# Performance work log

Hardware: AMD Instinct MI355X
Metric: run time of the kernel (lower is better)

The kernel has to match this reference:

```python
import jax, jax.numpy as jnp
import numpy as np

DIM = 64
NUM_NODES = 64
SEQ_LEN = 256
BATCH = 64


def setup_inputs() -> dict:
    key = jax.random.key(0)
    ks = jax.random.split(key, 8)
    D = DIM
    x = jax.random.normal(ks[0], (SEQ_LEN, BATCH, NUM_NODES, D), dtype=jnp.float32)
    mask = jnp.ones((SEQ_LEN,), dtype=jnp.int32)
    # msg MLP: Linear(3D -> D) + GELU
    lim_msg = 1.0 / np.sqrt(3 * D)
    msg_W = jax.random.uniform(ks[1], (D, 3 * D), minval=-lim_msg, maxval=lim_msg, dtype=jnp.float32)
    msg_b = jax.random.uniform(ks[2], (D,), minval=-lim_msg, maxval=lim_msg, dtype=jnp.float32)
    # GRUCell(input=D, hidden=D); torch init U(-1/sqrt(hidden), 1/sqrt(hidden))
    lim_g = 1.0 / np.sqrt(D)
    W_ih = jax.random.uniform(ks[3], (3 * D, D), minval=-lim_g, maxval=lim_g, dtype=jnp.float32)
    W_hh = jax.random.uniform(ks[4], (3 * D, D), minval=-lim_g, maxval=lim_g, dtype=jnp.float32)
    b_ih = jax.random.uniform(ks[5], (3 * D,), minval=-lim_g, maxval=lim_g, dtype=jnp.float32)
    b_hh = jax.random.uniform(ks[6], (3 * D,), minval=-lim_g, maxval=lim_g, dtype=jnp.float32)
    # TimeEncode params
    basis_freq = jnp.asarray(1.0 / 10.0 ** np.linspace(0, 9, D), dtype=jnp.float32)
    phase = jnp.zeros((D,), dtype=jnp.float32)
    return {"x": x, "mask": mask, "msg_W": msg_W, "msg_b": msg_b,
            "W_ih": W_ih, "W_hh": W_hh, "b_ih": b_ih, "b_hh": b_hh,
            "basis_freq": basis_freq, "phase": phase}


def _forward(x, mask, msg_W, msg_b, W_ih, W_hh, b_ih, b_hh, basis_freq, phase):
    T, B, C, D = x.shape
    # TimeEncode: cos(t * freq + phase) -> [T, D]
    ts = jnp.arange(T, dtype=jnp.float32)[:, None]
    t_enc = jnp.cos(ts * basis_freq[None, :] + phase[None, :])
    # init_func == 'mean': mean over time -> [B, C, D] -> [B*C, D]
    s0 = jnp.mean(x, axis=0).reshape(B * C, D)
    # time_range = arange(T) * mask (gather indices)
    tr = jnp.arange(T) * mask.astype(jnp.int32)
    x_seq = x[tr].reshape(T, B * C, D)      # gathered timesteps
    te_seq = t_enc[tr]                       # [T, D]

    def step(s, inp):
        xt, tt = inp                        # xt: [B*C, D], tt: [D]
        tt_b = jnp.broadcast_to(tt[None, :], xt.shape)
        cat = jnp.concatenate([xt, s, tt_b], axis=-1)  # [B*C, 3D]
        msg = jax.nn.gelu(cat @ msg_W.T + msg_b, approximate=False)
        # GRUCell (torch gate order: r, z, n)
        gi = msg @ W_ih.T + b_ih
        gh = s @ W_hh.T + b_hh
        i_r, i_z, i_n = jnp.split(gi, 3, axis=-1)
        h_r, h_z, h_n = jnp.split(gh, 3, axis=-1)
        r = jax.nn.sigmoid(i_r + h_r)
        z = jax.nn.sigmoid(i_z + h_z)
        n = jnp.tanh(i_n + r * h_n)
        s_new = (1.0 - z) * n + z * s
        return s_new, s_new

    _, states = jax.lax.scan(step, s0, (x_seq, te_seq))
    return states.reshape(T, B, C, D)


def reference(x, mask, msg_W, msg_b, W_ih, W_hh, b_ih, b_hh, basis_freq, phase):
    return _forward(x, mask, msg_W, msg_b, W_ih, W_hh, b_ih, b_hh, basis_freq, phase)
```

## Files before the change

### kernel.cpp

```cpp
#include <hip/hip_runtime.h>
#include <math.h>

#define DD    64
#define TT    256
#define NROW  4096
#define BLK   512
#define GRID  256

typedef __attribute__((ext_vector_type(8))) short  short8;
typedef __attribute__((ext_vector_type(4))) float  f32x4;

__device__ __forceinline__ unsigned short f2bf(float f) {
  unsigned u = __builtin_bit_cast(unsigned, f);
  u += 0x7fffu + ((u >> 16) & 1u);
  return (unsigned short)(u >> 16);
}

__device__ __forceinline__ unsigned long long pack4(float4 v) {
  return (unsigned long long)f2bf(v.x)
       | ((unsigned long long)f2bf(v.y) << 16)
       | ((unsigned long long)f2bf(v.z) << 32)
       | ((unsigned long long)f2bf(v.w) << 48);
}

__device__ __forceinline__ short8 load_wfrag(const float* p) {
  float4 a = *(const float4*)p;
  float4 b = *(const float4*)(p + 4);
  short8 r;
  r[0] = (short)f2bf(a.x); r[1] = (short)f2bf(a.y);
  r[2] = (short)f2bf(a.z); r[3] = (short)f2bf(a.w);
  r[4] = (short)f2bf(b.x); r[5] = (short)f2bf(b.y);
  r[6] = (short)f2bf(b.z); r[7] = (short)f2bf(b.w);
  return r;
}

__device__ __forceinline__ float fsigmoid(float x) {
  return __builtin_amdgcn_rcpf(1.0f + __expf(-x));
}
__device__ __forceinline__ float ftanh(float x) {
  return 1.0f - 2.0f * __builtin_amdgcn_rcpf(1.0f + __expf(2.0f * x));
}
__device__ __forceinline__ float ferf(float x) {
  float ax = fabsf(x);
  float t  = __builtin_amdgcn_rcpf(fmaf(0.3275911f, ax, 1.0f));
  float p  = fmaf(1.061405429f, t, -1.453152027f);
  p = fmaf(p, t, 1.421413741f);
  p = fmaf(p, t, -0.284496736f);
  p = fmaf(p, t, 0.254829592f);
  p = p * t;
  float y = 1.0f - p * __expf(-ax * ax);
  return copysignf(y, x);
}

__global__ void bias_kernel(const float* __restrict__ msg_W,
                            const float* __restrict__ msg_b,
                            const float* __restrict__ freq,
                            const float* __restrict__ phase,
                            float* __restrict__ bias_t) {
  __shared__ float teL[DD];
  const int t = blockIdx.x;
  const int j = threadIdx.x;
  teL[j] = cosf(fmaf((float)t, freq[j], phase[j]));
  __syncthreads();
  float acc = msg_b[j];
  const float* wrow = msg_W + j * 192 + 128;
  #pragma unroll 8
  for (int k = 0; k < DD; ++k) acc = fmaf(teL[k], wrow[k], acc);
  bias_t[t * DD + j] = acc;
}

__launch_bounds__(BLK, 1)
__global__ void scan4(const float* __restrict__ x,
                      const int*   __restrict__ mask,
                      const float* __restrict__ msg_W,
                      const float* __restrict__ W_ih,
                      const float* __restrict__ W_hh,
                      const float* __restrict__ b_ih,
                      const float* __restrict__ b_hh,
                      const float* __restrict__ bias_t,
                      float* __restrict__ out) {
  __shared__ alignas(16) unsigned short xs[16 * 72];
  __shared__ alignas(16) unsigned short ss[16 * 72];
  __shared__ alignas(16) unsigned short ms[16 * 72];
  __shared__ alignas(16) float s0a[16 * 68];
  __shared__ alignas(16) float ghl[16 * 260];
  __shared__ int tr_lds[TT];

  const int tid  = threadIdx.x;
  const int lane = tid & 63;
  const int wv   = tid >> 6;
  const int grp  = wv >> 2;
  const int w4   = wv & 3;
  const int col  = lane & 15;
  const int kh   = lane >> 4;
  const int n    = w4 * 16 + col;
  const int row0 = blockIdx.x * 16;

  if (tid < TT) tr_lds[tid] = tid * mask[tid];

  short8 wm[4], wi[3][2], wh[3][2];
  float bsum01[2] = {0.f, 0.f}, bih2 = 0.f, bhh2 = 0.f;
  if (grp == 0) {
    const float* mrow = msg_W + (size_t)n * 192;
    #pragma unroll
    for (int kf = 0; kf < 4; ++kf) wm[kf] = load_wfrag(mrow + kf * 32 + kh * 8);
    #pragma unroll
    for (int p = 0; p < 3; ++p) {
      const float* irow = W_ih + (size_t)(p * 64 + n) * 64;
      #pragma unroll
      for (int kf = 0; kf < 2; ++kf) wi[p][kf] = load_wfrag(irow + kf * 32 + kh * 8);
    }
    bsum01[0] = b_ih[n]      + b_hh[n];
    bsum01[1] = b_ih[64 + n] + b_hh[64 + n];
    bih2 = b_ih[128 + n];
    bhh2 = b_hh[128 + n];
  } else {
    #pragma unroll
    for (int p = 0; p < 3; ++p) {
      const float* hrow = W_hh + (size_t)(p * 64 + n) * 64;
      #pragma unroll
      for (int kf = 0; kf < 2; ++kf) wh[p][kf] = load_wfrag(hrow + kf * 32 + kh * 8);
    }
  }

  {
    const int half = tid >> 8, rem = tid & 255;
    const int fr = rem >> 4, fd = (rem & 15) * 4;
    const float* px = x + ((size_t)half * 128) * (NROW * DD)
                        + (size_t)(row0 + fr) * DD + fd;
    float4 acc = {0.f, 0.f, 0.f, 0.f};
    #pragma unroll 4
    for (int tl = 0; tl < 128; ++tl) {
      float4 v = *(const float4*)(px + (size_t)tl * (NROW * DD));
      acc.x += v.x; acc.y += v.y; acc.z += v.z; acc.w += v.w;
    }
    float* dst = (half == 0) ? &s0a[fr * 68 + fd] : &ghl[fr * 68 + fd];
    *(float4*)dst = acc;
  }
  __syncthreads();
  if (tid < 256) {
    const int fr = tid >> 4, fd = (tid & 15) * 4;
    float4 a = *(const float4*)&s0a[fr * 68 + fd];
    float4 b = *(const float4*)&ghl[fr * 68 + fd];
    const float inv = 1.0f / 256.0f;
    float4 m = { (a.x + b.x) * inv, (a.y + b.y) * inv,
                 (a.z + b.z) * inv, (a.w + b.w) * inv };
    *(float4*)&s0a[fr * 68 + fd] = m;
    *(unsigned long long*)&ss[fr * 72 + fd] = pack4(m);
    float4 xv0 = *(const float4*)(x + (size_t)(row0 + fr) * DD + fd);
    *(unsigned long long*)&xs[fr * 72 + fd] = pack4(xv0);
  }
  __syncthreads();

  float s_reg[4] = {0.f, 0.f, 0.f, 0.f};
  float btc = 0.f;
  if (grp == 0) {
    #pragma unroll
    for (int i = 0; i < 4; ++i) s_reg[i] = s0a[(kh * 4 + i) * 68 + n];
    btc = bias_t[n];
    __builtin_amdgcn_s_setprio(1);
  }

  const int t1  = tid & 255;
  const int fr1 = t1 >> 4;
  const int fd1 = (t1 & 15) * 4;
  float4 xv = {0.f, 0.f, 0.f, 0.f};

  for (int t = 0; t < TT; ++t) {
    const int tn = (t + 1 < TT) ? tr_lds[t + 1] : 0;
    if (grp == 0) {
      const unsigned short* ax = &xs[(lane & 15) * 72];
      const unsigned short* as = &ss[(lane & 15) * 72];
      short8 xa0 = *(const short8*)(ax + kh * 8);
      short8 xa1 = *(const short8*)(ax + 32 + kh * 8);
      short8 sa0 = *(const short8*)(as + kh * 8);
      short8 sa1 = *(const short8*)(as + 32 + kh * 8);
      f32x4 accm = {0.f, 0.f, 0.f, 0.f};
      accm = __builtin_amdgcn_mfma_f32_16x16x32_bf16(xa0, wm[0], accm, 0, 0, 0);
      accm = __builtin_amdgcn_mfma_f32_16x16x32_bf16(xa1, wm[1], accm, 0, 0, 0);
      accm = __builtin_amdgcn_mfma_f32_16x16x32_bf16(sa0, wm[2], accm, 0, 0, 0);
      accm = __builtin_amdgcn_mfma_f32_16x16x32_bf16(sa1, wm[3], accm, 0, 0, 0);
      float btn = 0.f;
      if (t + 1 < TT) btn = bias_t[tn * DD + n];
      #pragma unroll
      for (int i = 0; i < 4; ++i) {
        float a = accm[i] + btc;
        float g = 0.5f * a * (1.0f + ferf(a * 0.70710678118654752f));
        ms[(kh * 4 + i) * 72 + n] = f2bf(g);
      }
      btc = btn;
    } else {
      const unsigned short* as = &ss[(lane & 15) * 72];
      short8 sa0 = *(const short8*)(as + kh * 8);
      short8 sa1 = *(const short8*)(as + 32 + kh * 8);
      f32x4 agh[3];
      #pragma unroll
      for (int p = 0; p < 3; ++p) {
        f32x4 c = {0.f, 0.f, 0.f, 0.f};
        c = __builtin_amdgcn_mfma_f32_16x16x32_bf16(sa0, wh[p][0], c, 0, 0, 0);
        c = __builtin_amdgcn_mfma_f32_16x16x32_bf16(sa1, wh[p][1], c, 0, 0, 0);
        agh[p] = c;
      }
      #pragma unroll
      for (int i = 0; i < 4; ++i) {
        float4 gv = { agh[0][i], agh[1][i], agh[2][i], 0.f };
        *(float4*)&ghl[(kh * 4 + i) * 260 + n * 4] = gv;
      }
      if (t > 0) {
        float4 ov = *(const float4*)&s0a[fr1 * 68 + fd1];
        *(float4*)(out + ((size_t)(t - 1) * NROW + row0 + fr1) * DD + fd1) = ov;
      }
      if (t + 1 < TT)
        xv = *(const float4*)(x + ((size_t)tn * NROW + row0 + fr1) * DD + fd1);
    }
    __syncthreads();

    if (grp == 0) {
      const unsigned short* am = &ms[(lane & 15) * 72];
      short8 ma0 = *(const short8*)(am + kh * 8);
      short8 ma1 = *(const short8*)(am + 32 + kh * 8);
      f32x4 agi[3];
      #pragma unroll
      for (int p = 0; p < 3; ++p) {
        f32x4 c = {0.f, 0.f, 0.f, 0.f};
        c = __builtin_amdgcn_mfma_f32_16x16x32_bf16(ma0, wi[p][0], c, 0, 0, 0);
        c = __builtin_amdgcn_mfma_f32_16x16x32_bf16(ma1, wi[p][1], c, 0, 0, 0);
        agi[p] = c;
      }
      #pragma unroll
      for (int i = 0; i < 4; ++i) {
        const int rr = kh * 4 + i;
        float4 gh4 = *(const float4*)&ghl[rr * 260 + n * 4];
        float gr  = agi[0][i] + gh4.x + bsum01[0];
        float gz  = agi[1][i] + gh4.y + bsum01[1];
        float gni = agi[2][i] + bih2;
        float gnh = gh4.z + bhh2;
        float rg = fsigmoid(gr);
        float zg = fsigmoid(gz);
        float ng = ftanh(fmaf(rg, gnh, gni));
        float sn = fmaf(zg, s_reg[i] - ng, ng);
        s_reg[i] = sn;
        ss[rr * 72 + n]  = f2bf(sn);
        s0a[rr * 68 + n] = sn;
      }
    } else {
      if (t + 1 < TT)
        *(unsigned long long*)&xs[fr1 * 72 + fd1] = pack4(xv);
    }
    __syncthreads();
  }

  if (grp == 1) {
    float4 ov = *(const float4*)&s0a[fr1 * 68 + fd1];
    *(float4*)(out + ((size_t)(TT - 1) * NROW + row0 + fr1) * DD + fd1) = ov;
  }
}

extern "C" void kernel_launch(void* const* d_in, const int* in_sizes, int n_in,
                              void* d_out, int out_size, void* d_ws, size_t ws_size,
                              hipStream_t stream) {
  const float* x      = (const float*)d_in[0];
  const int*   mask   = (const int*)  d_in[1];
  const float* msg_W  = (const float*)d_in[2];
  const float* msg_b  = (const float*)d_in[3];
  const float* W_ih   = (const float*)d_in[4];
  const float* W_hh   = (const float*)d_in[5];
  const float* b_ih   = (const float*)d_in[6];
  const float* b_hh   = (const float*)d_in[7];
  const float* freq   = (const float*)d_in[8];
  const float* phase  = (const float*)d_in[9];
  float* out    = (float*)d_out;
  float* bias_t = (float*)d_ws;

  (void)in_sizes; (void)n_in; (void)out_size; (void)ws_size;

  bias_kernel<<<TT, DD, 0, stream>>>(msg_W, msg_b, freq, phase, bias_t);
  scan4<<<GRID, BLK, 0, stream>>>(x, mask, msg_W, W_ih, W_hh,
                                  b_ih, b_hh, bias_t, out);
}
```

Before: 305.2 us.

## Double-buffer x tile, prefetch two steps ahead, and use lgkm-only barriers

The x tile in shared memory becomes double-buffered so the helper wave group can write step t+1's tile and issue the global load for step t+2 before its recurrent matmul. The loop barriers are replaced by a custom barrier that waits only on LDS/scalar counters, so outstanding global loads and stores no longer stall each step. The output is now written directly from registers by the GRU waves instead of being staged through s0a and stored a step later. The message matmul is split into two independent accumulator chains to shorten the MFMA dependency chain. In exchange, the direct output stores are scalar per-lane writes, and correctness now depends on the manual waitcnt handling.

```diff
diff --git a/kernel.cpp b/kernel.cpp
--- a/kernel.cpp
+++ b/kernel.cpp
@@ -9,6 +9,13 @@
 
 typedef __attribute__((ext_vector_type(8))) short  short8;
 typedef __attribute__((ext_vector_type(4))) float  f32x4;
+
+#define BARRIER() do {                                        \
+    asm volatile("s_waitcnt lgkmcnt(0)" ::: "memory");        \
+    __builtin_amdgcn_sched_barrier(0);                        \
+    __builtin_amdgcn_s_barrier();                             \
+    __builtin_amdgcn_sched_barrier(0);                        \
+  } while (0)
 
 __device__ __forceinline__ unsigned short f2bf(float f) {
   unsigned u = __builtin_bit_cast(unsigned, f);
@@ -70,7 +77,7 @@
 }
 
 __launch_bounds__(BLK, 1)
-__global__ void scan4(const float* __restrict__ x,
+__global__ void scan5(const float* __restrict__ x,
                       const int*   __restrict__ mask,
                       const float* __restrict__ msg_W,
                       const float* __restrict__ W_ih,
@@ -79,12 +86,12 @@
                       const float* __restrict__ b_hh,
                       const float* __restrict__ bias_t,
                       float* __restrict__ out) {
-  __shared__ alignas(16) unsigned short xs[16 * 72];
+  __shared__ alignas(16) unsigned short xs[2][16 * 72];
   __shared__ alignas(16) unsigned short ss[16 * 72];
   __shared__ alignas(16) unsigned short ms[16 * 72];
   __shared__ alignas(16) float s0a[16 * 68];
   __shared__ alignas(16) float ghl[16 * 260];
-  __shared__ int tr_lds[TT];
+  __shared__ int tr_lds[TT + 2];
 
   const int tid  = threadIdx.x;
   const int lane = tid & 63;
@@ -97,6 +104,7 @@
   const int row0 = blockIdx.x * 16;
 
   if (tid < TT) tr_lds[tid] = tid * mask[tid];
+  else if (tid < TT + 2) tr_lds[tid] = 0;
 
   short8 wm[4], wi[3][2], wh[3][2];
   float bsum01[2] = {0.f, 0.f}, bih2 = 0.f, bhh2 = 0.f;
@@ -148,7 +156,7 @@
     *(float4*)&s0a[fr * 68 + fd] = m;
     *(unsigned long long*)&ss[fr * 72 + fd] = pack4(m);
     float4 xv0 = *(const float4*)(x + (size_t)(row0 + fr) * DD + fd);
-    *(unsigned long long*)&xs[fr * 72 + fd] = pack4(xv0);
+    *(unsigned long long*)&xs[0][fr * 72 + fd] = pack4(xv0);
   }
   __syncthreads();
 
@@ -165,31 +173,37 @@
   const int fr1 = t1 >> 4;
   const int fd1 = (t1 & 15) * 4;
   float4 xv = {0.f, 0.f, 0.f, 0.f};
+  if (grp == 1)
+    xv = *(const float4*)(x + ((size_t)tr_lds[1] * NROW + row0 + fr1) * DD + fd1);
 
   for (int t = 0; t < TT; ++t) {
-    const int tn = (t + 1 < TT) ? tr_lds[t + 1] : 0;
     if (grp == 0) {
-      const unsigned short* ax = &xs[(lane & 15) * 72];
+      const unsigned short* ax = &xs[t & 1][(lane & 15) * 72];
       const unsigned short* as = &ss[(lane & 15) * 72];
       short8 xa0 = *(const short8*)(ax + kh * 8);
       short8 xa1 = *(const short8*)(ax + 32 + kh * 8);
       short8 sa0 = *(const short8*)(as + kh * 8);
       short8 sa1 = *(const short8*)(as + 32 + kh * 8);
-      f32x4 accm = {0.f, 0.f, 0.f, 0.f};
-      accm = __builtin_amdgcn_mfma_f32_16x16x32_bf16(xa0, wm[0], accm, 0, 0, 0);
-      accm = __builtin_amdgcn_mfma_f32_16x16x32_bf16(xa1, wm[1], accm, 0, 0, 0);
-      accm = __builtin_amdgcn_mfma_f32_16x16x32_bf16(sa0, wm[2], accm, 0, 0, 0);
-      accm = __builtin_amdgcn_mfma_f32_16x16x32_bf16(sa1, wm[3], accm, 0, 0, 0);
       float btn = 0.f;
-      if (t + 1 < TT) btn = bias_t[tn * DD + n];
+      if (t + 1 < TT) btn = bias_t[tr_lds[t + 1] * DD + n];
+      f32x4 amx = {0.f, 0.f, 0.f, 0.f};
+      amx = __builtin_amdgcn_mfma_f32_16x16x32_bf16(xa0, wm[0], amx, 0, 0, 0);
+      amx = __builtin_amdgcn_mfma_f32_16x16x32_bf16(xa1, wm[1], amx, 0, 0, 0);
+      f32x4 ams = {0.f, 0.f, 0.f, 0.f};
+      ams = __builtin_amdgcn_mfma_f32_16x16x32_bf16(sa0, wm[2], ams, 0, 0, 0);
+      ams = __builtin_amdgcn_mfma_f32_16x16x32_bf16(sa1, wm[3], ams, 0, 0, 0);
       #pragma unroll
       for (int i = 0; i < 4; ++i) {
-        float a = accm[i] + btc;
+        float a = amx[i] + ams[i] + btc;
         float g = 0.5f * a * (1.0f + ferf(a * 0.70710678118654752f));
         ms[(kh * 4 + i) * 72 + n] = f2bf(g);
       }
       btc = btn;
     } else {
+      if (t + 1 < TT)
+        *(unsigned long long*)&xs[(t + 1) & 1][fr1 * 72 + fd1] = pack4(xv);
+      if (t + 2 < TT)
+        xv = *(const float4*)(x + ((size_t)tr_lds[t + 2] * NROW + row0 + fr1) * DD + fd1);
       const unsigned short* as = &ss[(lane & 15) * 72];
       short8 sa0 = *(const short8*)(as + kh * 8);
       short8 sa1 = *(const short8*)(as + 32 + kh * 8);
@@ -206,14 +220,8 @@
         float4 gv = { agh[0][i], agh[1][i], agh[2][i], 0.f };
         *(float4*)&ghl[(kh * 4 + i) * 260 + n * 4] = gv;
       }
-      if (t > 0) {
-        float4 ov = *(const float4*)&s0a[fr1 * 68 + fd1];
-        *(float4*)(out + ((size_t)(t - 1) * NROW + row0 + fr1) * DD + fd1) = ov;
-      }
-      if (t + 1 < TT)
-        xv = *(const float4*)(x + ((size_t)tn * NROW + row0 + fr1) * DD + fd1);
-    }
-    __syncthreads();
+    }
+    BARRIER();
 
     if (grp == 0) {
       const unsigned short* am = &ms[(lane & 15) * 72];
@@ -240,19 +248,11 @@
         float ng = ftanh(fmaf(rg, gnh, gni));
         float sn = fmaf(zg, s_reg[i] - ng, ng);
         s_reg[i] = sn;
-        ss[rr * 72 + n]  = f2bf(sn);
-        s0a[rr * 68 + n] = sn;
-      }
-    } else {
-      if (t + 1 < TT)
-        *(unsigned long long*)&xs[fr1 * 72 + fd1] = pack4(xv);
-    }
-    __syncthreads();
-  }
-
-  if (grp == 1) {
-    float4 ov = *(const float4*)&s0a[fr1 * 68 + fd1];
-    *(float4*)(out + ((size_t)(TT - 1) * NROW + row0 + fr1) * DD + fd1) = ov;
+        ss[rr * 72 + n] = f2bf(sn);
+        out[((size_t)t * NROW + row0 + rr) * DD + n] = sn;
+      }
+    }
+    BARRIER();
   }
 }
 
@@ -275,6 +275,6 @@
   (void)in_sizes; (void)n_in; (void)out_size; (void)ws_size;
 
   bias_kernel<<<TT, DD, 0, stream>>>(msg_W, msg_b, freq, phase, bias_t);
-  scan4<<<GRID, BLK, 0, stream>>>(x, mask, msg_W, W_ih, W_hh,
+  scan5<<<GRID, BLK, 0, stream>>>(x, mask, msg_W, W_ih, W_hh,
                                   b_ih, b_hh, bias_t, out);
 }
```

New measurement: 345.7 us. 13.3% more time.
